# Kernel tuning notes

Measured on AMD Instinct MI355X. Metric: run time of the kernel, lower is better.

The kernel has to match this reference:

```python
import jax, jax.numpy as jnp
import numpy as np

N = 100000      # nodes
E = 640000      # total edges across all relations
D_IN = 128
D_OUT = 128
R = 8           # num_rel
B = 4           # num_bases


def setup_inputs() -> dict:
    key = jax.random.key(0)
    ks = jax.random.split(key, 7)
    return {
        "X": jax.random.normal(ks[0], (N, D_IN), dtype=jnp.float32),
        "edge_src": jax.random.randint(ks[1], (E,), 0, N, dtype=jnp.int32),
        "edge_dst": jax.random.randint(ks[2], (E,), 0, N, dtype=jnp.int32),
        "edge_rel": jax.random.randint(ks[3], (E,), 0, R, dtype=jnp.int32),
        "edge_val": jax.random.uniform(ks[4], (E,), dtype=jnp.float32),
        "w_bases": jax.random.normal(ks[5], (B, D_IN, D_OUT), dtype=jnp.float32) * 0.05,
        "w_rel": jax.random.normal(ks[6], (R, B), dtype=jnp.float32) * 0.5,
    }


def reference(X, edge_src, edge_dst, edge_rel, edge_val, w_bases, w_rel):
    # Per-relation SpMM: support_r = A_r @ X, where A_r rows are destinations.
    # Fuse all relations into one gather + one segmented scatter-add.
    msg = X[edge_src] * edge_val[:, None]                      # [E, D_IN]
    seg = edge_rel.astype(jnp.int32) * N + edge_dst            # combined (rel, dst) id
    supports = jax.ops.segment_sum(msg, seg, num_segments=R * N)
    supports = supports.reshape(R, N, D_IN)                    # == concat of per-rel supports
    # Basis-decomposed relation weights: w[r] = sum_b w_rel[r,b] * w_bases[b]
    w = jnp.einsum("rb,bio->rio", w_rel, w_bases)              # [R, D_IN, D_OUT]
    # cat(supports, dim=1) @ w.view(R*D_IN, D_OUT) == sum_r supports_r @ w_r
    out = jnp.einsum("rni,rio->no", supports, w)               # [N, D_OUT]
    return out
```

## Files before the change

kernel.cpp:

```cpp
#include <hip/hip_runtime.h>
#include <stdint.h>

#define D_IN 128
#define D_OUT 128
#define NREL 8
#define NBASE 4

typedef __attribute__((ext_vector_type(8))) short short8;
typedef __attribute__((ext_vector_type(4))) float floatx4;
typedef __attribute__((ext_vector_type(2))) float floatx2;

__device__ __forceinline__ unsigned short f2bf(float f) {
  unsigned int u = __float_as_uint(f);
  u += 0x7fffu + ((u >> 16) & 1u);
  return (unsigned short)(u >> 16);
}
__device__ __forceinline__ unsigned pack2bf(float lo, float hi) {
  return (unsigned)f2bf(lo) | ((unsigned)f2bf(hi) << 16);
}
__device__ __forceinline__ float bflo(unsigned int u) { return __uint_as_float(u << 16); }
__device__ __forceinline__ float bfhi(unsigned int u) { return __uint_as_float(u & 0xffff0000u); }

__global__ void k_prep(const float4* __restrict__ X, ushort4* __restrict__ Xb, int n4,
                       const float* __restrict__ w_bases, unsigned short* __restrict__ W2T,
                       const int* __restrict__ edst, int* __restrict__ counts, int E) {
  int i = blockIdx.x * blockDim.x + threadIdx.x;
  if (i < n4) {
    float4 v = X[i];
    ushort4 o;
    o.x = f2bf(v.x); o.y = f2bf(v.y); o.z = f2bf(v.z); o.w = f2bf(v.w);
    Xb[i] = o;
  }
  if (i < 128 * 512) {
    int o = i >> 9, c = i & 511;
    int k = c >> 2, b = c & 3;
    W2T[i] = f2bf(w_bases[(b * D_IN + k) * D_OUT + o]);
  }
  if (i < E) atomicAdd(&counts[edst[i]], 1);
}

__global__ void k_scan1(const int* __restrict__ counts, int* __restrict__ localsc,
                        int* __restrict__ bsum, int Nn) {
  __shared__ int s[256];
  int i = blockIdx.x * 256 + threadIdx.x;
  int v = (i < Nn) ? counts[i] : 0;
  s[threadIdx.x] = v;
  __syncthreads();
  for (int off = 1; off < 256; off <<= 1) {
    int t = 0;
    if (threadIdx.x >= off) t = s[threadIdx.x - off];
    __syncthreads();
    s[threadIdx.x] += t;
    __syncthreads();
  }
  if (i < Nn) localsc[i] = s[threadIdx.x] - v;
  if (threadIdx.x == 255) bsum[blockIdx.x] = s[255];
}

__global__ void k_scan23(const int* __restrict__ localsc, const int* __restrict__ bsum,
                         int* __restrict__ offsets, int* __restrict__ cursor, int Nn, int E) {
  __shared__ int red[256];
  int acc = 0;
  for (int j = threadIdx.x; j < blockIdx.x; j += 256) acc += bsum[j];
  red[threadIdx.x] = acc;
  __syncthreads();
  for (int off = 128; off > 0; off >>= 1) {
    if (threadIdx.x < off) red[threadIdx.x] += red[threadIdx.x + off];
    __syncthreads();
  }
  int pref = red[0];
  int i = blockIdx.x * 256 + threadIdx.x;
  if (i < Nn) {
    int v = localsc[i] + pref;
    offsets[i] = v;
    cursor[i] = v;
  }
  if (i == 0) offsets[Nn] = E;
}

__global__ void k_bucket(const int* __restrict__ src, const int* __restrict__ dst,
                         const int* __restrict__ rel, const float* __restrict__ val,
                         int* __restrict__ cursor, uint2* __restrict__ bucket, int E) {
  int i = blockIdx.x * blockDim.x + threadIdx.x;
  if (i >= E) return;
  int d = dst[i];
  int pos = atomicAdd(&cursor[d], 1);
  bucket[pos] = make_uint2((unsigned)src[i] | ((unsigned)rel[i] << 21), __float_as_uint(val[i]));
}

__global__ __launch_bounds__(256, 4)
void k_agg_gemm(const uint2* __restrict__ bucket, const int* __restrict__ offsets,
                const float* __restrict__ w_rel_g, const unsigned* __restrict__ Xb2,
                const unsigned short* __restrict__ W2T, float* __restrict__ out, int Nn) {
  __shared__ __align__(16) unsigned short aggS[32][520];
  __shared__ __align__(16) float wrS[NREL * NBASE];
  if (threadIdx.x < NREL * NBASE) wrS[threadIdx.x] = w_rel_g[threadIdx.x];
  __syncthreads();

  const int wave = threadIdx.x >> 6, lane = threadIdx.x & 63;
  const int d0 = blockIdx.x * 32 + wave * 8;
  const unsigned* __restrict__ Xl = Xb2 + lane;
  const floatx2 zf2 = {0.f, 0.f};

  int oidx = d0 + (lane < 8 ? lane : 8);
  if (oidx > Nn) oidx = Nn;
  const int offv = offsets[oidx];
  const int s0 = __builtin_amdgcn_readlane(offv, 0);
  const int e8 = __builtin_amdgcn_readlane(offv, 8);

  floatx2 a0 = zf2, a1 = zf2, a2 = zf2, a3 = zf2;
  int row = 0;
  int bnd = __builtin_amdgcn_readlane(offv, 1);

#define FLUSH()                                                      \
  do {                                                               \
    uint4 o_;                                                        \
    o_.x = pack2bf(a0.x, a1.x);                                      \
    o_.y = pack2bf(a2.x, a3.x);                                      \
    o_.z = pack2bf(a0.y, a1.y);                                      \
    o_.w = pack2bf(a2.y, a3.y);                                      \
    *(uint4*)&aggS[wave * 8 + row][lane * 8] = o_;                   \
    a0 = zf2; a1 = zf2; a2 = zf2; a3 = zf2;                          \
    ++row;                                                           \
    bnd = (row < 8) ? __builtin_amdgcn_readlane(offv, row + 1)       \
                    : 0x7fffffff;                                    \
  } while (0)

#define ACCT(EI, R, V, Y)                                            \
  do {                                                               \
    if ((EI) < e8) {                                                 \
      while ((EI) == bnd) FLUSH();                                   \
      const float4 w_ = *(const float4*)&wrS[((R) >> 21) * 4];       \
      const float val_ = __uint_as_float(V);                         \
      const float c0_ = val_ * w_.x, c1_ = val_ * w_.y;              \
      const float c2_ = val_ * w_.z, c3_ = val_ * w_.w;              \
      floatx2 x_;                                                    \
      x_.x = bflo(Y);                                                \
      x_.y = bfhi(Y);                                                \
      a0 += c0_ * x_;                                                \
      a1 += c1_ * x_;                                                \
      a2 += c2_ * x_;                                                \
      a3 += c3_ * x_;                                                \
    }                                                                \
  } while (0)

#define LOADG(P, BASE)                                               \
  do {                                                               \
    int t0_ = (BASE); if (t0_ > ce) t0_ = ce;                        \
    if (t0_ - cbase >= 64) {                                         \
      cbase += 64;                                                   \
      chC = chN;                                                     \
      int in_ = cbase + 64 + lane;                                   \
      if (in_ > ce) in_ = ce;                                        \
      chN = bucket[in_];                                             \
    }                                                                \
    int t1_ = (BASE) + 1; if (t1_ > ce) t1_ = ce;                    \
    int t2_ = (BASE) + 2; if (t2_ > ce) t2_ = ce;                    \
    int t3_ = (BASE) + 3; if (t3_ > ce) t3_ = ce;                    \
    const int j0_ = t0_ - cbase, j1_ = t1_ - cbase;                  \
    const int j2_ = t2_ - cbase, j3_ = t3_ - cbase;                  \
    r##P##0 = __shfl(chC.x, j0_); v##P##0 = __shfl(chC.y, j0_);      \
    r##P##1 = __shfl(chC.x, j1_); v##P##1 = __shfl(chC.y, j1_);      \
    r##P##2 = __shfl(chC.x, j2_); v##P##2 = __shfl(chC.y, j2_);      \
    r##P##3 = __shfl(chC.x, j3_); v##P##3 = __shfl(chC.y, j3_);      \
    y##P##0 = Xl[(r##P##0 & 0x1FFFFFu) << 6];                        \
    y##P##1 = Xl[(r##P##1 & 0x1FFFFFu) << 6];                        \
    y##P##2 = Xl[(r##P##2 & 0x1FFFFFu) << 6];                        \
    y##P##3 = Xl[(r##P##3 & 0x1FFFFFu) << 6];                        \
  } while (0)

  if (s0 < e8) {
    const int ce = e8 - 1;
    int cbase = s0;
    uint2 chC, chN;
    {
      int i0 = cbase + lane;
      if (i0 > ce) i0 = ce;
      chC = bucket[i0];
      int i1 = cbase + 64 + lane;
      if (i1 > ce) i1 = ce;
      chN = bucket[i1];
    }
    unsigned rA0, rA1, rA2, rA3, vA0, vA1, vA2, vA3, yA0, yA1, yA2, yA3;
    unsigned rB0, rB1, rB2, rB3, vB0, vB1, vB2, vB3, yB0, yB1, yB2, yB3;
    unsigned rC0, rC1, rC2, rC3, vC0, vC1, vC2, vC3, yC0, yC1, yC2, yC3;
    unsigned rD0, rD1, rD2, rD3, vD0, vD1, vD2, vD3, yD0, yD1, yD2, yD3;
    LOADG(A, s0);
    LOADG(B, s0 + 4);
    LOADG(C, s0 + 8);
    int gi = s0;
    while (gi < e8) {
      LOADG(D, gi + 12);
      ACCT(gi, rA0, vA0, yA0);
      ACCT(gi + 1, rA1, vA1, yA1);
      ACCT(gi + 2, rA2, vA2, yA2);
      ACCT(gi + 3, rA3, vA3, yA3);
      LOADG(A, gi + 16);
      ACCT(gi + 4, rB0, vB0, yB0);
      ACCT(gi + 5, rB1, vB1, yB1);
      ACCT(gi + 6, rB2, vB2, yB2);
      ACCT(gi + 7, rB3, vB3, yB3);
      LOADG(B, gi + 20);
      ACCT(gi + 8, rC0, vC0, yC0);
      ACCT(gi + 9, rC1, vC1, yC1);
      ACCT(gi + 10, rC2, vC2, yC2);
      ACCT(gi + 11, rC3, vC3, yC3);
      LOADG(C, gi + 24);
      ACCT(gi + 12, rD0, vD0, yD0);
      ACCT(gi + 13, rD1, vD1, yD1);
      ACCT(gi + 14, rD2, vD2, yD2);
      ACCT(gi + 15, rD3, vD3, yD3);
      gi += 16;
    }
  }
  while (row < 8) FLUSH();

  __syncthreads();

  const int q = lane >> 4, r16 = lane & 15;
  const int wn = wave * 32;
  const floatx4 zero = {0.f, 0.f, 0.f, 0.f};
  floatx4 acc[2][2];
  acc[0][0] = zero; acc[0][1] = zero; acc[1][0] = zero; acc[1][1] = zero;

#pragma unroll 4
  for (int k0 = 0; k0 < 512; k0 += 32) {
    int ka = k0 + q * 8;
    short8 af[2], bfv[2];
    af[0] = *(const short8*)&aggS[r16][ka];
    af[1] = *(const short8*)&aggS[16 + r16][ka];
    bfv[0] = *(const short8*)(W2T + (size_t)(wn + r16) * 512 + ka);
    bfv[1] = *(const short8*)(W2T + (size_t)(wn + 16 + r16) * 512 + ka);
#pragma unroll
    for (int i = 0; i < 2; ++i)
#pragma unroll
      for (int j = 0; j < 2; ++j)
        acc[i][j] = __builtin_amdgcn_mfma_f32_16x16x32_bf16(af[i], bfv[j], acc[i][j], 0, 0, 0);
  }

#pragma unroll
  for (int i = 0; i < 2; ++i) {
#pragma unroll
    for (int j = 0; j < 2; ++j) {
#pragma unroll
      for (int p = 0; p < 4; ++p) {
        int prow = i * 16 + q * 4 + p;
        int col = wn + j * 16 + r16;
        int grow = blockIdx.x * 32 + prow;
        if (grow < Nn) out[(size_t)grow * 128 + col] = acc[i][j][p];
      }
    }
  }
}

extern "C" void kernel_launch(void* const* d_in, const int* in_sizes, int n_in,
                              void* d_out, int out_size, void* d_ws, size_t ws_size,
                              hipStream_t stream) {
  const float* X = (const float*)d_in[0];
  const int* esrc = (const int*)d_in[1];
  const int* edst = (const int*)d_in[2];
  const int* erel = (const int*)d_in[3];
  const float* eval_ = (const float*)d_in[4];
  const float* w_bases = (const float*)d_in[5];
  const float* w_rel = (const float*)d_in[6];
  const int Nn = in_sizes[0] / D_IN;
  const int E = in_sizes[1];

  char* ws = (char*)d_ws;
  size_t off = 0;
  auto alloc = [&](size_t bytes) -> char* {
    char* p = ws + off;
    off += (bytes + 255) & ~(size_t)255;
    return p;
  };
  unsigned short* Xb = (unsigned short*)alloc((size_t)Nn * D_IN * 2);
  unsigned short* W2T = (unsigned short*)alloc((size_t)128 * 512 * 2);
  int* counts = (int*)alloc((size_t)Nn * 4);
  int* cursor = (int*)alloc((size_t)Nn * 4);
  int* offsets = (int*)alloc((size_t)(Nn + 1) * 4);
  int* localsc = (int*)alloc((size_t)Nn * 4);
  int* bsum = (int*)alloc(4096);
  uint2* bucket = (uint2*)alloc((size_t)E * 8);
  (void)ws_size;

  int n4 = Nn * D_IN / 4;
  hipMemsetAsync(counts, 0, (size_t)Nn * 4, stream);
  k_prep<<<(n4 + 255) / 256, 256, 0, stream>>>((const float4*)X, (ushort4*)Xb, n4,
                                               w_bases, W2T, edst, counts, E);

  int nb = (Nn + 255) / 256;
  k_scan1<<<nb, 256, 0, stream>>>(counts, localsc, bsum, Nn);
  k_scan23<<<nb, 256, 0, stream>>>(localsc, bsum, offsets, cursor, Nn, E);
  k_bucket<<<(E + 255) / 256, 256, 0, stream>>>(esrc, edst, erel, eval_, cursor, bucket, E);

  k_agg_gemm<<<(Nn + 31) / 32, 256, 0, stream>>>(bucket, offsets, w_rel,
                                                 (const unsigned*)Xb, W2T,
                                                 (float*)d_out, Nn);
}
```

Measured before the change: 254.9 us.

## Merge preprocessing kernels into one cooperative kernel with grid syncs

Replaces the memset, prep, two scan kernels and bucket kernel with a single cooperative launch of 1024 blocks that separates the phases with grid.sync(), which removes several launch gaps. It also packs the relation id into the low 3 bits of the edge value, so the aggregation loop no longer needs to mask the source index and carries fewer registers. The cost is that the value loses 3 mantissa bits. The scan assumes Nn is at most 1024*256 and the grid must be co-resident, and the grid-stride loops now run with far fewer threads than the old per-element launches.

```diff
diff --git a/kernel.cpp b/kernel.cpp
--- a/kernel.cpp
+++ b/kernel.cpp
@@ -1,10 +1,14 @@
 #include <hip/hip_runtime.h>
+#include <hip/hip_cooperative_groups.h>
 #include <stdint.h>
+
+namespace cg = cooperative_groups;
 
 #define D_IN 128
 #define D_OUT 128
 #define NREL 8
 #define NBASE 4
+#define NBLK 1024
 
 typedef __attribute__((ext_vector_type(8))) short short8;
 typedef __attribute__((ext_vector_type(4))) float floatx4;
@@ -21,29 +25,38 @@
 __device__ __forceinline__ float bflo(unsigned int u) { return __uint_as_float(u << 16); }
 __device__ __forceinline__ float bfhi(unsigned int u) { return __uint_as_float(u & 0xffff0000u); }
 
-__global__ void k_prep(const float4* __restrict__ X, ushort4* __restrict__ Xb, int n4,
-                       const float* __restrict__ w_bases, unsigned short* __restrict__ W2T,
-                       const int* __restrict__ edst, int* __restrict__ counts, int E) {
-  int i = blockIdx.x * blockDim.x + threadIdx.x;
-  if (i < n4) {
+__global__ __launch_bounds__(256)
+void k_build(const float4* __restrict__ X, ushort4* __restrict__ Xb, int n4,
+             const float* __restrict__ w_bases, unsigned short* __restrict__ W2T,
+             const int* __restrict__ esrc, const int* __restrict__ edst,
+             const int* __restrict__ erel, const float* __restrict__ eval_,
+             int* __restrict__ counts, int* __restrict__ offsets,
+             int* __restrict__ cursor, int* __restrict__ bsum,
+             int* __restrict__ bpre, uint2* __restrict__ bucket, int Nn, int E) {
+  cg::grid_group grid = cg::this_grid();
+  const int tid = blockIdx.x * 256 + threadIdx.x;
+  const int nth = NBLK * 256;
+  __shared__ int s[256];
+
+  const int ncu4 = (Nn + 3) >> 2;
+  for (int i = tid; i < ncu4; i += nth) ((uint4*)counts)[i] = make_uint4(0u, 0u, 0u, 0u);
+  for (int i = tid; i < n4; i += nth) {
     float4 v = X[i];
     ushort4 o;
     o.x = f2bf(v.x); o.y = f2bf(v.y); o.z = f2bf(v.z); o.w = f2bf(v.w);
     Xb[i] = o;
   }
-  if (i < 128 * 512) {
+  for (int i = tid; i < 128 * 512; i += nth) {
     int o = i >> 9, c = i & 511;
     int k = c >> 2, b = c & 3;
     W2T[i] = f2bf(w_bases[(b * D_IN + k) * D_OUT + o]);
   }
-  if (i < E) atomicAdd(&counts[edst[i]], 1);
-}
-
-__global__ void k_scan1(const int* __restrict__ counts, int* __restrict__ localsc,
-                        int* __restrict__ bsum, int Nn) {
-  __shared__ int s[256];
-  int i = blockIdx.x * 256 + threadIdx.x;
-  int v = (i < Nn) ? counts[i] : 0;
+  grid.sync();
+
+  for (int i = tid; i < E; i += nth) atomicAdd(&counts[edst[i]], 1);
+  grid.sync();
+
+  int v = (tid < Nn) ? counts[tid] : 0;
   s[threadIdx.x] = v;
   __syncthreads();
   for (int off = 1; off < 256; off <<= 1) {
@@ -53,39 +66,46 @@
     s[threadIdx.x] += t;
     __syncthreads();
   }
-  if (i < Nn) localsc[i] = s[threadIdx.x] - v;
-  if (threadIdx.x == 255) bsum[blockIdx.x] = s[255];
-}
-
-__global__ void k_scan23(const int* __restrict__ localsc, const int* __restrict__ bsum,
-                         int* __restrict__ offsets, int* __restrict__ cursor, int Nn, int E) {
-  __shared__ int red[256];
-  int acc = 0;
-  for (int j = threadIdx.x; j < blockIdx.x; j += 256) acc += bsum[j];
-  red[threadIdx.x] = acc;
-  __syncthreads();
-  for (int off = 128; off > 0; off >>= 1) {
-    if (threadIdx.x < off) red[threadIdx.x] += red[threadIdx.x + off];
+  const int locincl = s[threadIdx.x];
+  if (threadIdx.x == 255) bsum[blockIdx.x] = locincl;
+  grid.sync();
+
+  if (blockIdx.x == 0) {
+    const int base = threadIdx.x * 4;
+    int b0 = bsum[base], b1 = bsum[base + 1], b2 = bsum[base + 2], b3 = bsum[base + 3];
+    int tsum = b0 + b1 + b2 + b3;
+    s[threadIdx.x] = tsum;
     __syncthreads();
-  }
-  int pref = red[0];
-  int i = blockIdx.x * 256 + threadIdx.x;
-  if (i < Nn) {
-    int v = localsc[i] + pref;
-    offsets[i] = v;
-    cursor[i] = v;
-  }
-  if (i == 0) offsets[Nn] = E;
-}
-
-__global__ void k_bucket(const int* __restrict__ src, const int* __restrict__ dst,
-                         const int* __restrict__ rel, const float* __restrict__ val,
-                         int* __restrict__ cursor, uint2* __restrict__ bucket, int E) {
-  int i = blockIdx.x * blockDim.x + threadIdx.x;
-  if (i >= E) return;
-  int d = dst[i];
-  int pos = atomicAdd(&cursor[d], 1);
-  bucket[pos] = make_uint2((unsigned)src[i] | ((unsigned)rel[i] << 21), __float_as_uint(val[i]));
+    for (int off = 1; off < 256; off <<= 1) {
+      int t = 0;
+      if (threadIdx.x >= off) t = s[threadIdx.x - off];
+      __syncthreads();
+      s[threadIdx.x] += t;
+      __syncthreads();
+    }
+    int excl = s[threadIdx.x] - tsum;
+    bpre[base] = excl;
+    bpre[base + 1] = excl + b0;
+    bpre[base + 2] = excl + b0 + b1;
+    bpre[base + 3] = excl + b0 + b1 + b2;
+  }
+  grid.sync();
+
+  const int pre = bpre[blockIdx.x];
+  if (tid < Nn) {
+    int o = pre + locincl - v;
+    offsets[tid] = o;
+    cursor[tid] = o;
+  }
+  if (tid == 0) offsets[Nn] = E;
+  grid.sync();
+
+  for (int i = tid; i < E; i += nth) {
+    int d = edst[i];
+    int pos = atomicAdd(&cursor[d], 1);
+    unsigned vr = (__float_as_uint(eval_[i]) & ~7u) | (unsigned)erel[i];
+    bucket[pos] = make_uint2((unsigned)esrc[i], vr);
+  }
 }
 
 __global__ __launch_bounds__(256, 4)
@@ -126,12 +146,12 @@
                     : 0x7fffffff;                                    \
   } while (0)
 
-#define ACCT(EI, R, V, Y)                                            \
+#define ACCT(EI, V, Y)                                               \
   do {                                                               \
     if ((EI) < e8) {                                                 \
       while ((EI) == bnd) FLUSH();                                   \
-      const float4 w_ = *(const float4*)&wrS[((R) >> 21) * 4];       \
-      const float val_ = __uint_as_float(V);                         \
+      const float4 w_ = *(const float4*)&wrS[((V) & 7u) * 4];        \
+      const float val_ = __uint_as_float((V) & ~7u);                 \
       const float c0_ = val_ * w_.x, c1_ = val_ * w_.y;              \
       const float c2_ = val_ * w_.z, c3_ = val_ * w_.w;              \
       floatx2 x_;                                                    \
@@ -159,14 +179,14 @@
     int t3_ = (BASE) + 3; if (t3_ > ce) t3_ = ce;                    \
     const int j0_ = t0_ - cbase, j1_ = t1_ - cbase;                  \
     const int j2_ = t2_ - cbase, j3_ = t3_ - cbase;                  \
-    r##P##0 = __shfl(chC.x, j0_); v##P##0 = __shfl(chC.y, j0_);      \
-    r##P##1 = __shfl(chC.x, j1_); v##P##1 = __shfl(chC.y, j1_);      \
-    r##P##2 = __shfl(chC.x, j2_); v##P##2 = __shfl(chC.y, j2_);      \
-    r##P##3 = __shfl(chC.x, j3_); v##P##3 = __shfl(chC.y, j3_);      \
-    y##P##0 = Xl[(r##P##0 & 0x1FFFFFu) << 6];                        \
-    y##P##1 = Xl[(r##P##1 & 0x1FFFFFu) << 6];                        \
-    y##P##2 = Xl[(r##P##2 & 0x1FFFFFu) << 6];                        \
-    y##P##3 = Xl[(r##P##3 & 0x1FFFFFu) << 6];                        \
+    unsigned g0_ = __shfl(chC.x, j0_); v##P##0 = __shfl(chC.y, j0_); \
+    unsigned g1_ = __shfl(chC.x, j1_); v##P##1 = __shfl(chC.y, j1_); \
+    unsigned g2_ = __shfl(chC.x, j2_); v##P##2 = __shfl(chC.y, j2_); \
+    unsigned g3_ = __shfl(chC.x, j3_); v##P##3 = __shfl(chC.y, j3_); \
+    y##P##0 = Xl[g0_ << 6];                                          \
+    y##P##1 = Xl[g1_ << 6];                                          \
+    y##P##2 = Xl[g2_ << 6];                                          \
+    y##P##3 = Xl[g3_ << 6];                                          \
   } while (0)
 
   if (s0 < e8) {
@@ -181,35 +201,35 @@
       if (i1 > ce) i1 = ce;
       chN = bucket[i1];
     }
-    unsigned rA0, rA1, rA2, rA3, vA0, vA1, vA2, vA3, yA0, yA1, yA2, yA3;
-    unsigned rB0, rB1, rB2, rB3, vB0, vB1, vB2, vB3, yB0, yB1, yB2, yB3;
-    unsigned rC0, rC1, rC2, rC3, vC0, vC1, vC2, vC3, yC0, yC1, yC2, yC3;
-    unsigned rD0, rD1, rD2, rD3, vD0, vD1, vD2, vD3, yD0, yD1, yD2, yD3;
+    unsigned vA0, vA1, vA2, vA3, yA0, yA1, yA2, yA3;
+    unsigned vB0, vB1, vB2, vB3, yB0, yB1, yB2, yB3;
+    unsigned vC0, vC1, vC2, vC3, yC0, yC1, yC2, yC3;
+    unsigned vD0, vD1, vD2, vD3, yD0, yD1, yD2, yD3;
     LOADG(A, s0);
     LOADG(B, s0 + 4);
     LOADG(C, s0 + 8);
     int gi = s0;
     while (gi < e8) {
       LOADG(D, gi + 12);
-      ACCT(gi, rA0, vA0, yA0);
-      ACCT(gi + 1, rA1, vA1, yA1);
-      ACCT(gi + 2, rA2, vA2, yA2);
-      ACCT(gi + 3, rA3, vA3, yA3);
+      ACCT(gi, vA0, yA0);
+      ACCT(gi + 1, vA1, yA1);
+      ACCT(gi + 2, vA2, yA2);
+      ACCT(gi + 3, vA3, yA3);
       LOADG(A, gi + 16);
-      ACCT(gi + 4, rB0, vB0, yB0);
-      ACCT(gi + 5, rB1, vB1, yB1);
-      ACCT(gi + 6, rB2, vB2, yB2);
-      ACCT(gi + 7, rB3, vB3, yB3);
+      ACCT(gi + 4, vB0, yB0);
+      ACCT(gi + 5, vB1, yB1);
+      ACCT(gi + 6, vB2, yB2);
+      ACCT(gi + 7, vB3, yB3);
       LOADG(B, gi + 20);
-      ACCT(gi + 8, rC0, vC0, yC0);
-      ACCT(gi + 9, rC1, vC1, yC1);
-      ACCT(gi + 10, rC2, vC2, yC2);
-      ACCT(gi + 11, rC3, vC3, yC3);
+      ACCT(gi + 8, vC0, yC0);
+      ACCT(gi + 9, vC1, yC1);
+      ACCT(gi + 10, vC2, yC2);
+      ACCT(gi + 11, vC3, yC3);
       LOADG(C, gi + 24);
-      ACCT(gi + 12, rD0, vD0, yD0);
-      ACCT(gi + 13, rD1, vD1, yD1);
-      ACCT(gi + 14, rD2, vD2, yD2);
-      ACCT(gi + 15, rD3, vD3, yD3);
+      ACCT(gi + 12, vD0, yD0);
+      ACCT(gi + 13, vD1, yD1);
+      ACCT(gi + 14, vD2, yD2);
+      ACCT(gi + 15, vD3, yD3);
       gi += 16;
     }
   }
@@ -263,8 +283,8 @@
   const float* eval_ = (const float*)d_in[4];
   const float* w_bases = (const float*)d_in[5];
   const float* w_rel = (const float*)d_in[6];
-  const int Nn = in_sizes[0] / D_IN;
-  const int E = in_sizes[1];
+  int Nn = in_sizes[0] / D_IN;
+  int E = in_sizes[1];
 
   char* ws = (char*)d_ws;
   size_t off = 0;
@@ -275,23 +295,22 @@
   };
   unsigned short* Xb = (unsigned short*)alloc((size_t)Nn * D_IN * 2);
   unsigned short* W2T = (unsigned short*)alloc((size_t)128 * 512 * 2);
-  int* counts = (int*)alloc((size_t)Nn * 4);
+  int* counts = (int*)alloc((size_t)(Nn + 4) * 4);
   int* cursor = (int*)alloc((size_t)Nn * 4);
   int* offsets = (int*)alloc((size_t)(Nn + 1) * 4);
-  int* localsc = (int*)alloc((size_t)Nn * 4);
-  int* bsum = (int*)alloc(4096);
+  int* bsum = (int*)alloc((size_t)NBLK * 4);
+  int* bpre = (int*)alloc((size_t)NBLK * 4);
   uint2* bucket = (uint2*)alloc((size_t)E * 8);
   (void)ws_size;
 
   int n4 = Nn * D_IN / 4;
-  hipMemsetAsync(counts, 0, (size_t)Nn * 4, stream);
-  k_prep<<<(n4 + 255) / 256, 256, 0, stream>>>((const float4*)X, (ushort4*)Xb, n4,
-                                               w_bases, W2T, edst, counts, E);
-
-  int nb = (Nn + 255) / 256;
-  k_scan1<<<nb, 256, 0, stream>>>(counts, localsc, bsum, Nn);
-  k_scan23<<<nb, 256, 0, stream>>>(localsc, bsum, offsets, cursor, Nn, E);
-  k_bucket<<<(E + 255) / 256, 256, 0, stream>>>(esrc, edst, erel, eval_, cursor, bucket, E);
+
+  const float4* X4 = (const float4*)X;
+  ushort4* Xb4 = (ushort4*)Xb;
+  void* args[] = {&X4, &Xb4, &n4, &w_bases, &W2T, &esrc, &edst, &erel, &eval_,
+                  &counts, &offsets, &cursor, &bsum, &bpre, &bucket, &Nn, &E};
+  hipLaunchCooperativeKernel(reinterpret_cast<void*>(k_build), dim3(NBLK), dim3(256),
+                             args, 0, stream);
 
   k_agg_gemm<<<(Nn + 31) / 32, 256, 0, stream>>>(bucket, offsets, w_rel,
                                                  (const unsigned*)Xb, W2T,
```

New measurement: 783.6 us. +207.4%, slower.
